# Optimization experiments

Measured on AMD Instinct MI355X. Metric: run time of the kernel, lower is better.

## Reference

```python
import jax, jax.numpy as jnp
import numpy as np

B, N, F, NCG, NCONV, VOCAB = 16, 1024, 128, 64, 3, 100
EPS = 0.001


def setup_inputs() -> dict:
    key = jax.random.key(0)
    ks = jax.random.split(key, 16)
    atoms_nodes = jax.random.randint(ks[0], (B, N), 0, VOCAB, dtype=jnp.int32)
    xyz = jax.random.normal(ks[1], (B, N, 3), jnp.float32) * 3.0
    # chain bonds (i, i+1) per molecule -> every atom has degree >= 1
    bi = jnp.repeat(jnp.arange(B), N - 1)
    si = jnp.tile(jnp.arange(N - 1), B)
    bonds = jnp.stack([bi, si, si + 1], axis=1).astype(jnp.int32)  # [B*(N-1), 3]
    tau = jnp.float32(1.0)
    gumbel_u = jax.random.uniform(ks[2], (B, N, NCG), jnp.float32, 1e-6, 1.0 - 1e-6)
    # parameters
    emb = jax.random.normal(ks[3], (VOCAB, F), jnp.float32) * 0.1
    emb = emb.at[0].set(0.0)  # padding_idx=0
    s = 1.0 / np.sqrt(F)
    upd_W1 = jax.random.uniform(ks[4], (NCONV, F, F), jnp.float32, -s, s)
    upd_b1 = jax.random.uniform(ks[5], (NCONV, F), jnp.float32, -s, s)
    upd_W2 = jax.random.uniform(ks[6], (NCONV, F, F), jnp.float32, -s, s)
    upd_b2 = jax.random.uniform(ks[7], (NCONV, F), jnp.float32, -s, s)
    cg_W1 = jax.random.uniform(ks[8], (F, F), jnp.float32, -s, s)
    cg_b1 = jax.random.uniform(ks[9], (F,), jnp.float32, -s, s)
    cg_W2 = jax.random.uniform(ks[10], (F, NCG), jnp.float32, -s, s)
    cg_b2 = jax.random.uniform(ks[11], (NCG,), jnp.float32, -s, s)
    return {"atoms_nodes": atoms_nodes, "xyz": xyz, "bonds": bonds, "tau": tau,
            "gumbel_u": gumbel_u, "emb": emb,
            "upd_W1": upd_W1, "upd_b1": upd_b1, "upd_W2": upd_W2, "upd_b2": upd_b2,
            "cg_W1": cg_W1, "cg_b1": cg_b1, "cg_W2": cg_W2, "cg_b2": cg_b2}


def reference(atoms_nodes, xyz, bonds, tau, gumbel_u, emb,
              upd_W1, upd_b1, upd_W2, upd_b2, cg_W1, cg_b1, cg_W2, cg_b2):
    h = emb[atoms_nodes]  # [B,N,F]
    # dense symmetric adjacency from bond list
    adj = jnp.zeros((B, N, N), jnp.float32)
    adj = adj.at[bonds[:, 0], bonds[:, 1], bonds[:, 2]].set(1.0)
    adj = adj.at[bonds[:, 0], bonds[:, 2], bonds[:, 1]].set(1.0)
    deg = jnp.sum(adj, axis=-1)[:, :, None]  # [B,N,1]
    for l in range(NCONV):
        ch = jnp.tanh(h @ upd_W1[l] + upd_b1[l]) @ upd_W2[l] + upd_b2[l]
        dh = jnp.einsum('bif,bij->bjf', ch, adj) / deg
        h = h + dh
    # gumbel-softmax assignment (soft)
    assign_logits = jnp.tanh(h @ cg_W1 + cg_b1) @ cg_W2 + cg_b2  # [B,N,NCG]
    g = -jnp.log(-jnp.log(gumbel_u))
    M = jax.nn.softmax((assign_logits + g) / tau, axis=-1)  # [B,N,NCG]
    M_norm = M / jnp.sum(M, axis=-2, keepdims=True)
    H = jnp.einsum('bnj,bnf->bjf', M_norm, h)        # [B,NCG,F]
    cg_xyz = jnp.einsum('bin,bij->bjn', xyz, M_norm)  # [B,NCG,3]
    cg_adj = jnp.broadcast_to(jnp.ones((NCG, NCG)) - jnp.eye(NCG), (B, NCG, NCG))
    diff = cg_xyz[:, :, None, :] - cg_xyz[:, None, :, :]
    dist = jnp.sqrt(jnp.sum(diff * diff, axis=-1) + EPS)  # [B,NCG,NCG]
    knbrs = jnp.argsort(dist, axis=-1)
    return (M, M_norm, h, H, adj, cg_xyz, cg_adj, knbrs)
```

## Files before the change

kernel.cpp:

```cpp
#include <hip/hip_runtime.h>
#include <math.h>

#define BB 16
#define NN 1024
#define FF 128
#define NCG 64
#define NCONV 3
#define CAP 8

static const size_t O_M     = 0;
static const size_t O_MN    = (size_t)BB*NN*NCG;
static const size_t O_H     = O_MN  + (size_t)BB*NN*NCG;
static const size_t O_HH    = O_H   + (size_t)BB*NN*FF;
static const size_t O_ADJ   = O_HH  + (size_t)BB*NCG*FF;
static const size_t O_CGXYZ = O_ADJ + (size_t)BB*NN*NN;
static const size_t O_CGADJ = O_CGXYZ + (size_t)BB*NCG*3;
static const size_t O_KN    = O_CGADJ + (size_t)BB*NCG*NCG;

static const size_t S_H64   = 0;
static const size_t S_T64   = 2097152;
static const size_t S_C64   = 4194304;
static const size_t S_LM64  = 0;
static const size_t S_COLSP = 4194304;
static const size_t S_HPF   = 6291456;
static const size_t S_CGP   = 6815744;
static const size_t S_NBR   = 6840320;
static const size_t S_W64   = 6905856;

static const size_t WO_CGW1 = 98304;
static const size_t WO_CGW2 = 114688;
static const int    W64_N   = 122880;

static const size_t W_INVD = 0;
static const size_t W_COLS = (size_t)BB*NN;
static const size_t W_CG64 = W_COLS + (size_t)BB*NCG;
static const size_t W_CNT  = W_CG64 + (size_t)BB*NCG*3;

__global__ void k_zero(int* cnt) {
    int i = blockIdx.x * blockDim.x + threadIdx.x;
    if (i < BB*NN) cnt[i] = 0;
}

__global__ void k_build_nbr(const int* __restrict__ bonds, int nb, int* cnt, int* nbr) {
    int i = blockIdx.x * blockDim.x + threadIdx.x;
    if (i >= nb) return;
    int b = bonds[i*3+0], s = bonds[i*3+1], t = bonds[i*3+2];
    int ns = b*NN + s, nt = b*NN + t;
    int p = atomicAdd(&cnt[ns], 1);
    if (p < CAP) nbr[(size_t)ns*CAP + p] = nt;
    int q = atomicAdd(&cnt[nt], 1);
    if (q < CAP) nbr[(size_t)nt*CAP + q] = ns;
}

__global__ void k_invdeg(const int* __restrict__ cnt, double* invdeg) {
    int i = blockIdx.x * blockDim.x + threadIdx.x;
    if (i >= BB*NN) return;
    int d = cnt[i];
    invdeg[i] = d > 0 ? 1.0 / (double)d : 0.0;
}

__global__ void k_cgadj(float* cgadj) {
    int idx = blockIdx.x * blockDim.x + threadIdx.x;
    if (idx >= BB*NCG*NCG) return;
    int i = (idx / NCG) % NCG, j = idx % NCG;
    cgadj[idx] = (i == j) ? 0.f : 1.f;
}

__global__ void k_emb64(const int* __restrict__ atoms, const float* __restrict__ emb,
                        double* __restrict__ h) {
    int idx = blockIdx.x * blockDim.x + threadIdx.x;
    if (idx >= BB*NN*(FF/4)) return;
    int n = idx / (FF/4), f4 = idx % (FF/4);
    int a = atoms[n];
    const float4 v = *reinterpret_cast<const float4*>(&emb[(size_t)a*FF + f4*4]);
    double* hp = &h[(size_t)n*FF + f4*4];
    hp[0] = (double)v.x; hp[1] = (double)v.y; hp[2] = (double)v.z; hp[3] = (double)v.w;
}

__global__ void k_cvtW(const float* __restrict__ uW1, const float* __restrict__ uW2,
                       const float* __restrict__ cgW1, const float* __restrict__ cgW2,
                       double* __restrict__ W64) {
    int idx = blockIdx.x * blockDim.x + threadIdx.x;
    if (idx >= W64_N) return;
    float v;
    if (idx < 98304) {
        int l = idx >> 15, r = idx & 32767;
        v = (r < 16384) ? uW1[l*16384 + r] : uW2[l*16384 + (r & 16383)];
    } else if (idx < 114688) {
        v = cgW1[idx - 98304];
    } else {
        v = cgW2[idx - 114688];
    }
    W64[idx] = (double)v;
}

template<int COUTT, bool TANH>
__global__ __launch_bounds__(256) void k_gemm64(const double* __restrict__ in,
                                                const double* __restrict__ W,
                                                const float* __restrict__ bias,
                                                double* __restrict__ out) {
    constexpr int K = 128, KC = 32;
    constexpr int CT2 = COUTT/2;
    __shared__ double As[64*34];
    __shared__ double Ws[KC*64];
    const int tid = threadIdx.x;
    const int col0 = blockIdx.y * 64;
    const int C02 = col0 >> 1;
    const size_t row0 = (size_t)blockIdx.x * 64;
    const double2* in2 = reinterpret_cast<const double2*>(in + row0*K);
    const double2* Wg2 = reinterpret_cast<const double2*>(W);
    double2* As2 = reinterpret_cast<double2*>(As);
    double2* Ws2 = reinterpret_cast<double2*>(Ws);

    double2 pA[4], pW[4];
    #pragma unroll
    for (int i = 0; i < 4; ++i) { int q = tid + i*256; pA[i] = in2[(q>>4)*64 + (q&15)]; }
    #pragma unroll
    for (int i = 0; i < 4; ++i) { int q = tid + i*256; pW[i] = Wg2[(q>>5)*CT2 + C02 + (q&31)]; }

    const int tc = tid & 15, tr = tid >> 4;
    double acc[4][4];
    #pragma unroll
    for (int i = 0; i < 4; ++i)
        #pragma unroll
        for (int j = 0; j < 4; ++j) acc[i][j] = 0.0;

    for (int kc = 0; kc < K; kc += KC) {
        __syncthreads();
        #pragma unroll
        for (int i = 0; i < 4; ++i) { int q = tid + i*256; As2[(q>>4)*17 + (q&15)] = pA[i]; }
        #pragma unroll
        for (int i = 0; i < 4; ++i) { int q = tid + i*256; Ws2[(q>>5)*32 + (q&31)] = pW[i]; }
        if (kc + KC < K) {
            const int kn = kc + KC, kn2 = kn >> 1;
            #pragma unroll
            for (int i = 0; i < 4; ++i) { int q = tid + i*256; pA[i] = in2[(q>>4)*64 + kn2 + (q&15)]; }
            #pragma unroll
            for (int i = 0; i < 4; ++i) { int q = tid + i*256; pW[i] = Wg2[(kn + (q>>5))*CT2 + C02 + (q&31)]; }
        }
        __syncthreads();
        #pragma unroll
        for (int kk2 = 0; kk2 < KC/2; ++kk2) {
            double2 a[4];
            #pragma unroll
            for (int i = 0; i < 4; ++i) a[i] = As2[(tr + 16*i)*17 + kk2];
            const double2* w0 = Ws2 + (2*kk2+0)*32;
            const double2* w1 = Ws2 + (2*kk2+1)*32;
            #pragma unroll
            for (int g = 0; g < 2; ++g) {
                double2 u0 = w0[tc + g*16];
                double2 u1 = w1[tc + g*16];
                #pragma unroll
                for (int i = 0; i < 4; ++i) {
                    acc[i][g*2+0] += a[i].x*u0.x + a[i].y*u1.x;
                    acc[i][g*2+1] += a[i].x*u0.y + a[i].y*u1.y;
                }
            }
        }
    }

    #pragma unroll
    for (int g = 0; g < 2; ++g) {
        int c = col0 + tc*2 + g*32;
        double b0 = (double)bias[c], b1 = (double)bias[c+1];
        #pragma unroll
        for (int i = 0; i < 4; ++i) {
            double2 o;
            o.x = acc[i][g*2+0] + b0;
            o.y = acc[i][g*2+1] + b1;
            if (TANH) { o.x = tanh(o.x); o.y = tanh(o.y); }
            *reinterpret_cast<double2*>(&out[(row0 + tr + 16*i)*COUTT + c]) = o;
        }
    }
}

template<bool WRITE_F32>
__global__ void k_gather(const double* __restrict__ ch, const double* __restrict__ invdeg,
                         const int* __restrict__ nbr, const int* __restrict__ cnt,
                         double* __restrict__ h, float* __restrict__ hout) {
    int idx = blockIdx.x * blockDim.x + threadIdx.x;
    if (idx >= BB*NN*(FF/4)) return;
    int node = idx >> 5, f4 = idx & 31;
    int c = cnt[node];
    double2 s0; s0.x = 0.0; s0.y = 0.0;
    double2 s1 = s0;
    for (int q = 0; q < c; ++q) {
        int nb = nbr[(size_t)node*CAP + q];
        const double2* cp = reinterpret_cast<const double2*>(ch + (size_t)nb*FF + f4*4);
        double2 a = cp[0], b2 = cp[1];
        s0.x += a.x; s0.y += a.y; s1.x += b2.x; s1.y += b2.y;
    }
    double w = invdeg[node];
    double2* hp = reinterpret_cast<double2*>(h + (size_t)node*FF + f4*4);
    double2 h0 = hp[0], h1 = hp[1];
    h0.x += s0.x*w; h0.y += s0.y*w; h1.x += s1.x*w; h1.y += s1.y*w;
    hp[0] = h0; hp[1] = h1;
    if (WRITE_F32) {
        float4 o; o.x = (float)h0.x; o.y = (float)h0.y; o.z = (float)h1.x; o.w = (float)h1.y;
        *reinterpret_cast<float4*>(&hout[(size_t)node*FF + f4*4]) = o;
    }
}

__global__ void k_softmax64(double* __restrict__ lm, const float* __restrict__ gum,
                            const float* __restrict__ tau_p, float* __restrict__ M_out) {
    int row = blockIdx.x * 4 + threadIdx.x / 64;
    int lane = threadIdx.x & 63;
    double tau = (double)(*tau_p);
    double u = (double)gum[(size_t)row*NCG + lane];
    double g = -log(-log(u));
    double v = (lm[(size_t)row*NCG + lane] + g) / tau;
    double m = v;
    #pragma unroll
    for (int off = 32; off; off >>= 1) m = fmax(m, __shfl_xor(m, off));
    double e = exp(v - m);
    double s = e;
    #pragma unroll
    for (int off = 32; off; off >>= 1) s += __shfl_xor(s, off);
    double mv = e / s;
    lm[(size_t)row*NCG + lane] = mv;
    M_out[(size_t)row*NCG + lane] = (float)mv;
}

__global__ __launch_bounds__(256) void k_cols_part(const double* __restrict__ M,
                                                   double* __restrict__ colsp) {
    __shared__ double red[256];
    const int b = blockIdx.x, c = blockIdx.y;
    const int tid = threadIdx.x;
    const int j = tid & 63, q = tid >> 6;
    const double* Mb = M + (size_t)b*NN*NCG + (size_t)(c*64 + q*16)*NCG;
    double s = 0.0;
    #pragma unroll
    for (int r = 0; r < 16; ++r) s += Mb[(size_t)r*NCG + j];
    red[tid] = s;
    __syncthreads();
    if (tid < 64)
        colsp[((size_t)b*16 + c)*NCG + j] = red[j] + red[64+j] + red[128+j] + red[192+j];
}

__global__ void k_cols_fin(const double* __restrict__ colsp, double* __restrict__ colsum) {
    int idx = blockIdx.x * blockDim.x + threadIdx.x;
    if (idx >= BB*NCG) return;
    int b = idx >> 6, j = idx & 63;
    double s = 0.0;
    #pragma unroll
    for (int c = 0; c < 16; ++c) s += colsp[((size_t)b*16 + c)*NCG + j];
    colsum[idx] = s;
}

__global__ void k_mnorm_out(const double* __restrict__ M, const double* __restrict__ colsum,
                            float* __restrict__ Mn) {
    size_t i = (size_t)blockIdx.x * blockDim.x + threadIdx.x;
    if (i >= (size_t)BB*NN*NCG) return;
    size_t b = i >> 16;
    int j = (int)(i & 63);
    Mn[i] = (float)(M[i] / colsum[b*NCG + j]);
}

__global__ __launch_bounds__(256) void k_Hpart32(const float* __restrict__ Mn,
                                                 const float* __restrict__ h,
                                                 float* __restrict__ Hp) {
    __shared__ float Ms[32*NCG];
    __shared__ float hs[32*FF];
    const int b = blockIdx.x, ch = blockIdx.y;
    const int tid = threadIdx.x;
    const int tc = tid % 32, tr = tid / 32;
    const float4* M4 = reinterpret_cast<const float4*>(Mn + (size_t)b*NN*NCG);
    const float4* h4 = reinterpret_cast<const float4*>(h + (size_t)b*NN*FF);
    float4* Ms4 = reinterpret_cast<float4*>(Ms);
    float4* hs4 = reinterpret_cast<float4*>(hs);
    const float2* Ms2 = reinterpret_cast<const float2*>(Ms);
    const float2* hs2 = reinterpret_cast<const float2*>(hs);

    float acc[8][4];
    #pragma unroll
    for (int i = 0; i < 8; ++i)
        #pragma unroll
        for (int j = 0; j < 4; ++j) acc[i][j] = 0.f;

    for (int s = 0; s < 4; ++s) {
        const int n0 = ch*128 + s*32;
        __syncthreads();
        #pragma unroll
        for (int i = 0; i < 2; ++i) Ms4[tid + i*256] = M4[n0*16 + tid + i*256];
        #pragma unroll
        for (int i = 0; i < 4; ++i) hs4[tid + i*256] = h4[n0*32 + tid + i*256];
        __syncthreads();
        for (int n = 0; n < 32; ++n) {
            float2 hv0 = hs2[n*64 + tc];
            float2 hv1 = hs2[n*64 + 32 + tc];
            float2 m0 = Ms2[n*32 + tr];
            float2 m1 = Ms2[n*32 + 8 + tr];
            float2 m2 = Ms2[n*32 + 16 + tr];
            float2 m3 = Ms2[n*32 + 24 + tr];
            float mj[8] = {m0.x, m0.y, m1.x, m1.y, m2.x, m2.y, m3.x, m3.y};
            #pragma unroll
            for (int jj = 0; jj < 8; ++jj) {
                acc[jj][0] += mj[jj]*hv0.x; acc[jj][1] += mj[jj]*hv0.y;
                acc[jj][2] += mj[jj]*hv1.x; acc[jj][3] += mj[jj]*hv1.y;
            }
        }
    }
    float* Ho = Hp + ((size_t)ch*BB + b) * NCG * FF;
    #pragma unroll
    for (int gj = 0; gj < 4; ++gj)
        #pragma unroll
        for (int pj = 0; pj < 2; ++pj) {
            int j = tr*2 + gj*16 + pj;
            int jj = gj*2 + pj;
            float2 o0; o0.x = acc[jj][0]; o0.y = acc[jj][1];
            float2 o1; o1.x = acc[jj][2]; o1.y = acc[jj][3];
            float2* op = reinterpret_cast<float2*>(Ho + (size_t)j*FF);
            op[tc] = o0; op[32 + tc] = o1;
        }
}

__global__ void k_Hfin32(const float* __restrict__ Hp, float* __restrict__ H) {
    int idx = blockIdx.x * blockDim.x + threadIdx.x;
    if (idx >= BB*NCG*FF) return;
    int b = idx / (NCG*FF);
    int r = idx % (NCG*FF);
    float s = 0.f;
    #pragma unroll
    for (int c = 0; c < 8; ++c) s += Hp[((size_t)c*BB + b)*NCG*FF + r];
    H[idx] = s;
}

__global__ __launch_bounds__(192) void k_cgpart(const double* __restrict__ M,
                                                const float* __restrict__ xyz,
                                                double* __restrict__ cgp) {
    __shared__ double Ms[32*NCG];
    __shared__ double xs[32*3];
    const int b = blockIdx.x, ch = blockIdx.y;
    const int tid = threadIdx.x;
    const int j = tid / 3, d = tid % 3;
    const double2* M2 = reinterpret_cast<const double2*>(M + (size_t)b*NN*NCG);
    double2* Ms2 = reinterpret_cast<double2*>(Ms);
    const float* xb = xyz + (size_t)b*NN*3;
    double acc = 0.0;
    for (int s = 0; s < 4; ++s) {
        const int n0 = ch*128 + s*32;
        __syncthreads();
        for (int q = tid; q < 1024; q += 192) Ms2[q] = M2[n0*32 + q];
        for (int q = tid; q < 96; q += 192) xs[q] = (double)xb[n0*3 + q];
        __syncthreads();
        for (int n = 0; n < 32; ++n)
            acc += Ms[n*NCG + j] * xs[n*3 + d];
    }
    cgp[((size_t)ch*BB + b)*NCG*3 + tid] = acc;
}

__global__ void k_cgfin(const double* __restrict__ cgp, const double* __restrict__ colsum,
                        double* __restrict__ cg64, float* __restrict__ cg) {
    int idx = blockIdx.x * blockDim.x + threadIdx.x;
    if (idx >= BB*NCG*3) return;
    int b = idx / (NCG*3);
    int r = idx % (NCG*3);
    int j = r / 3;
    double s = 0.0;
    #pragma unroll
    for (int c = 0; c < 8; ++c) s += cgp[((size_t)c*BB + b)*NCG*3 + r];
    double v = s / colsum[b*NCG + j];
    cg64[idx] = v;
    cg[idx] = (float)v;
}

__global__ __launch_bounds__(1024) void k_knbrs(const double* __restrict__ cg,
                                                float* __restrict__ kn) {
    __shared__ double cs[NCG*3];
    const int b = blockIdx.x;
    const int tid = threadIdx.x;
    const int i = blockIdx.y * 16 + tid / 64;
    const int j = tid & 63;
    if (tid < NCG*3) cs[tid] = cg[(size_t)b*NCG*3 + tid];
    __syncthreads();
    double xi = cs[i*3+0], yi = cs[i*3+1], zi = cs[i*3+2];
    double dxj = xi - cs[j*3+0], dyj = yi - cs[j*3+1], dzj = zi - cs[j*3+2];
    double d2j = dxj*dxj + dyj*dyj + dzj*dzj;
    int rank = 0;
    for (int k = 0; k < NCG; ++k) {
        double dx = xi - cs[k*3+0], dy = yi - cs[k*3+1], dz = zi - cs[k*3+2];
        double d2k = dx*dx + dy*dy + dz*dz;
        rank += (d2k < d2j) || (d2k == d2j && k < j);
    }
    kn[(size_t)b*NCG*NCG + (size_t)i*NCG + rank] = (float)j;
}

__global__ void k_zero_adj(float4* adj4, long n4) {
    long i = (long)blockIdx.x * blockDim.x + threadIdx.x;
    long stride = (long)gridDim.x * blockDim.x;
    float4 z; z.x = z.y = z.z = z.w = 0.f;
    for (; i < n4; i += stride) adj4[i] = z;
}

__global__ void k_bonds_adj(const int* __restrict__ bonds, int nb, float* adj) {
    int i = blockIdx.x * blockDim.x + threadIdx.x;
    if (i >= nb) return;
    int b = bonds[i*3+0], s = bonds[i*3+1], t = bonds[i*3+2];
    size_t base = (size_t)b * NN * NN;
    adj[base + (size_t)s*NN + t] = 1.f;
    adj[base + (size_t)t*NN + s] = 1.f;
}

extern "C" void kernel_launch(void* const* d_in, const int* in_sizes, int n_in,
                              void* d_out, int out_size, void* d_ws, size_t ws_size,
                              hipStream_t stream) {
    const int*   atoms  = (const int*)  d_in[0];
    const float* xyz    = (const float*)d_in[1];
    const int*   bonds  = (const int*)  d_in[2];
    const float* tau    = (const float*)d_in[3];
    const float* gum    = (const float*)d_in[4];
    const float* emb    = (const float*)d_in[5];
    const float* uW1    = (const float*)d_in[6];
    const float* ub1    = (const float*)d_in[7];
    const float* uW2    = (const float*)d_in[8];
    const float* ub2    = (const float*)d_in[9];
    const float* cgW1   = (const float*)d_in[10];
    const float* cgb1   = (const float*)d_in[11];
    const float* cgW2   = (const float*)d_in[12];
    const float* cgb2   = (const float*)d_in[13];

    float* out = (float*)d_out;
    float* o_M   = out + O_M;
    float* o_Mn  = out + O_MN;
    float* o_h   = out + O_H;
    float* o_H   = out + O_HH;
    float* o_adj = out + O_ADJ;
    float* o_cg  = out + O_CGXYZ;
    float* o_ca  = out + O_CGADJ;
    float* o_kn  = out + O_KN;

    double* scr   = (double*)o_adj;
    double* h64   = scr + S_H64;
    double* t64   = scr + S_T64;
    double* c64   = scr + S_C64;
    double* lm64  = scr + S_LM64;
    double* colsp = scr + S_COLSP;
    float*  Hpf   = (float*)(scr + S_HPF);
    double* cgp   = scr + S_CGP;
    int*    nbr   = (int*)(scr + S_NBR);
    double* W64   = scr + S_W64;

    double* wsd    = (double*)d_ws;
    double* invdeg = wsd + W_INVD;
    double* colsum = wsd + W_COLS;
    double* cg64   = wsd + W_CG64;
    int*    cnt    = (int*)(wsd + W_CNT);

    const int nb = in_sizes[2] / 3;

    hipLaunchKernelGGL(k_zero, dim3(64), dim3(256), 0, stream, cnt);
    hipLaunchKernelGGL(k_build_nbr, dim3((nb+255)/256), dim3(256), 0, stream,
                       bonds, nb, cnt, nbr);
    hipLaunchKernelGGL(k_invdeg, dim3(64), dim3(256), 0, stream, cnt, invdeg);
    hipLaunchKernelGGL(k_cgadj, dim3(256), dim3(256), 0, stream, o_ca);
    hipLaunchKernelGGL(k_cvtW, dim3((W64_N+255)/256), dim3(256), 0, stream,
                       uW1, uW2, cgW1, cgW2, W64);
    hipLaunchKernelGGL(k_emb64, dim3(2048), dim3(256), 0, stream, atoms, emb, h64);

    for (int l = 0; l < NCONV; ++l) {
        hipLaunchKernelGGL((k_gemm64<128,true>), dim3(256,2), dim3(256), 0, stream,
                           h64, W64 + (size_t)l*32768, ub1 + (size_t)l*FF, t64);
        hipLaunchKernelGGL((k_gemm64<128,false>), dim3(256,2), dim3(256), 0, stream,
                           t64, W64 + (size_t)l*32768 + 16384, ub2 + (size_t)l*FF, c64);
        if (l < NCONV-1)
            hipLaunchKernelGGL((k_gather<false>), dim3(2048), dim3(256), 0, stream,
                               c64, invdeg, nbr, cnt, h64, o_h);
        else
            hipLaunchKernelGGL((k_gather<true>), dim3(2048), dim3(256), 0, stream,
                               c64, invdeg, nbr, cnt, h64, o_h);
    }

    hipLaunchKernelGGL((k_gemm64<128,true>), dim3(256,2), dim3(256), 0, stream,
                       h64, W64 + WO_CGW1, cgb1, t64);
    hipLaunchKernelGGL((k_gemm64<64,false>), dim3(256,1), dim3(256), 0, stream,
                       t64, W64 + WO_CGW2, cgb2, lm64);

    hipLaunchKernelGGL(k_softmax64, dim3(4096), dim3(256), 0, stream,
                       lm64, gum, tau, o_M);
    hipLaunchKernelGGL(k_cols_part, dim3(16,16), dim3(256), 0, stream, lm64, colsp);
    hipLaunchKernelGGL(k_cols_fin, dim3(4), dim3(256), 0, stream, colsp, colsum);
    hipLaunchKernelGGL(k_mnorm_out, dim3(4096), dim3(256), 0, stream, lm64, colsum, o_Mn);
    hipLaunchKernelGGL(k_Hpart32, dim3(BB, 8), dim3(256), 0, stream, o_Mn, o_h, Hpf);
    hipLaunchKernelGGL(k_Hfin32, dim3(512), dim3(256), 0, stream, Hpf, o_H);
    hipLaunchKernelGGL(k_cgpart, dim3(BB, 8), dim3(192), 0, stream, lm64, xyz, cgp);
    hipLaunchKernelGGL(k_cgfin, dim3(12), dim3(256), 0, stream, cgp, colsum, cg64, o_cg);
    hipLaunchKernelGGL(k_knbrs, dim3(BB, 4), dim3(1024), 0, stream, cg64, o_kn);

    hipLaunchKernelGGL(k_zero_adj, dim3(4096), dim3(256), 0, stream,
                       (float4*)o_adj, (long)BB*NN*NN/4);
    hipLaunchKernelGGL(k_bonds_adj, dim3((nb+255)/256), dim3(256), 0, stream,
                       bonds, nb, o_adj);
}
```

Before: 399.8 us.

## Use FP64 MFMA for dense GEMMs and widen split-K for H and cg_xyz

Replaces the scalar FP64 register-tiled GEMM with a kernel built on the 16x16x4 FP64 MFMA instruction, padding the weight tile in shared memory to reduce bank conflicts. The k_Hpart32 reduction and cg_xyz partial-sum kernels are split over more node chunks (16 and 32), with more blocks per kernel and longer final reductions; scratch offsets move to fit the larger partial buffers. The aim is to raise GEMM throughput and fill more CUs in the small reduction kernels, at the cost of more partial-sum traffic and scalar rather than vector output stores.

```diff
diff --git a/kernel.cpp b/kernel.cpp
--- a/kernel.cpp
+++ b/kernel.cpp
@@ -7,6 +7,8 @@
 #define NCG 64
 #define NCONV 3
 #define CAP 8
+
+typedef double f64x4 __attribute__((ext_vector_type(4)));
 
 static const size_t O_M     = 0;
 static const size_t O_MN    = (size_t)BB*NN*NCG;
@@ -23,9 +25,9 @@
 static const size_t S_LM64  = 0;
 static const size_t S_COLSP = 4194304;
 static const size_t S_HPF   = 6291456;
-static const size_t S_CGP   = 6815744;
-static const size_t S_NBR   = 6840320;
-static const size_t S_W64   = 6905856;
+static const size_t S_CGP   = 7340032;
+static const size_t S_NBR   = 7438336;
+static const size_t S_W64   = 7503872;
 
 static const size_t WO_CGW1 = 98304;
 static const size_t WO_CGW2 = 114688;
@@ -95,14 +97,14 @@
 }
 
 template<int COUTT, bool TANH>
-__global__ __launch_bounds__(256) void k_gemm64(const double* __restrict__ in,
-                                                const double* __restrict__ W,
-                                                const float* __restrict__ bias,
-                                                double* __restrict__ out) {
+__global__ __launch_bounds__(256) void k_gemm_mfma(const double* __restrict__ in,
+                                                   const double* __restrict__ W,
+                                                   const float* __restrict__ bias,
+                                                   double* __restrict__ out) {
     constexpr int K = 128, KC = 32;
     constexpr int CT2 = COUTT/2;
     __shared__ double As[64*34];
-    __shared__ double Ws[KC*64];
+    __shared__ double Ws[KC*66];
     const int tid = threadIdx.x;
     const int col0 = blockIdx.y * 64;
     const int C02 = col0 >> 1;
@@ -118,19 +120,21 @@
     #pragma unroll
     for (int i = 0; i < 4; ++i) { int q = tid + i*256; pW[i] = Wg2[(q>>5)*CT2 + C02 + (q&31)]; }
 
-    const int tc = tid & 15, tr = tid >> 4;
-    double acc[4][4];
-    #pragma unroll
-    for (int i = 0; i < 4; ++i)
-        #pragma unroll
-        for (int j = 0; j < 4; ++j) acc[i][j] = 0.0;
+    const int lane = tid & 63;
+    const int wv = tid >> 6;
+    const int m = lane & 15, kq = lane >> 4;
+    const int arow = (wv*16 + m)*34 + kq;
+
+    f64x4 acc[4];
+    #pragma unroll
+    for (int ct = 0; ct < 4; ++ct) acc[ct] = (f64x4){0.0, 0.0, 0.0, 0.0};
 
     for (int kc = 0; kc < K; kc += KC) {
         __syncthreads();
         #pragma unroll
         for (int i = 0; i < 4; ++i) { int q = tid + i*256; As2[(q>>4)*17 + (q&15)] = pA[i]; }
         #pragma unroll
-        for (int i = 0; i < 4; ++i) { int q = tid + i*256; Ws2[(q>>5)*32 + (q&31)] = pW[i]; }
+        for (int i = 0; i < 4; ++i) { int q = tid + i*256; Ws2[(q>>5)*33 + (q&31)] = pW[i]; }
         if (kc + KC < K) {
             const int kn = kc + KC, kn2 = kn >> 1;
             #pragma unroll
@@ -140,36 +144,27 @@
         }
         __syncthreads();
         #pragma unroll
-        for (int kk2 = 0; kk2 < KC/2; ++kk2) {
-            double2 a[4];
+        for (int kk = 0; kk < KC; kk += 4) {
+            double a = As[arow + kk];
+            const double* wrow = Ws + (kk + kq)*66 + m;
             #pragma unroll
-            for (int i = 0; i < 4; ++i) a[i] = As2[(tr + 16*i)*17 + kk2];
-            const double2* w0 = Ws2 + (2*kk2+0)*32;
-            const double2* w1 = Ws2 + (2*kk2+1)*32;
-            #pragma unroll
-            for (int g = 0; g < 2; ++g) {
-                double2 u0 = w0[tc + g*16];
-                double2 u1 = w1[tc + g*16];
-                #pragma unroll
-                for (int i = 0; i < 4; ++i) {
-                    acc[i][g*2+0] += a[i].x*u0.x + a[i].y*u1.x;
-                    acc[i][g*2+1] += a[i].x*u0.y + a[i].y*u1.y;
-                }
+            for (int ct = 0; ct < 4; ++ct) {
+                double b = wrow[ct*16];
+                acc[ct] = __builtin_amdgcn_mfma_f64_16x16x4f64(a, b, acc[ct], 0, 0, 0);
             }
         }
     }
 
-    #pragma unroll
-    for (int g = 0; g < 2; ++g) {
-        int c = col0 + tc*2 + g*32;
-        double b0 = (double)bias[c], b1 = (double)bias[c+1];
+    const int orow = wv*16 + kq*4;
+    #pragma unroll
+    for (int ct = 0; ct < 4; ++ct) {
+        int c = col0 + ct*16 + m;
+        double bv = (double)bias[c];
         #pragma unroll
         for (int i = 0; i < 4; ++i) {
-            double2 o;
-            o.x = acc[i][g*2+0] + b0;
-            o.y = acc[i][g*2+1] + b1;
-            if (TANH) { o.x = tanh(o.x); o.y = tanh(o.y); }
-            *reinterpret_cast<double2*>(&out[(row0 + tr + 16*i)*COUTT + c]) = o;
+            double v = acc[ct][i] + bv;
+            if (TANH) v = tanh(v);
+            out[(row0 + orow + i)*COUTT + c] = v;
         }
     }
 }
@@ -277,8 +272,8 @@
         #pragma unroll
         for (int j = 0; j < 4; ++j) acc[i][j] = 0.f;
 
-    for (int s = 0; s < 4; ++s) {
-        const int n0 = ch*128 + s*32;
+    for (int s = 0; s < 2; ++s) {
+        const int n0 = ch*64 + s*32;
         __syncthreads();
         #pragma unroll
         for (int i = 0; i < 2; ++i) Ms4[tid + i*256] = M4[n0*16 + tid + i*256];
@@ -321,7 +316,7 @@
     int r = idx % (NCG*FF);
     float s = 0.f;
     #pragma unroll
-    for (int c = 0; c < 8; ++c) s += Hp[((size_t)c*BB + b)*NCG*FF + r];
+    for (int c = 0; c < 16; ++c) s += Hp[((size_t)c*BB + b)*NCG*FF + r];
     H[idx] = s;
 }
 
@@ -333,20 +328,17 @@
     const int b = blockIdx.x, ch = blockIdx.y;
     const int tid = threadIdx.x;
     const int j = tid / 3, d = tid % 3;
+    const int n0 = ch*32;
     const double2* M2 = reinterpret_cast<const double2*>(M + (size_t)b*NN*NCG);
     double2* Ms2 = reinterpret_cast<double2*>(Ms);
     const float* xb = xyz + (size_t)b*NN*3;
+    for (int q = tid; q < 1024; q += 192) Ms2[q] = M2[n0*32 + q];
+    for (int q = tid; q < 96; q += 192) xs[q] = (double)xb[n0*3 + q];
+    __syncthreads();
     double acc = 0.0;
-    for (int s = 0; s < 4; ++s) {
-        const int n0 = ch*128 + s*32;
-        __syncthreads();
-        for (int q = tid; q < 1024; q += 192) Ms2[q] = M2[n0*32 + q];
-        for (int q = tid; q < 96; q += 192) xs[q] = (double)xb[n0*3 + q];
-        __syncthreads();
-        for (int n = 0; n < 32; ++n)
-            acc += Ms[n*NCG + j] * xs[n*3 + d];
-    }
-    cgp[((size_t)ch*BB + b)*NCG*3 + tid] = acc;
+    #pragma unroll 8
+    for (int n = 0; n < 32; ++n) acc += Ms[n*NCG + j] * xs[n*3 + d];
+    cgp[((size_t)ch*BB + b)*192 + tid] = acc;
 }
 
 __global__ void k_cgfin(const double* __restrict__ cgp, const double* __restrict__ colsum,
@@ -358,7 +350,7 @@
     int j = r / 3;
     double s = 0.0;
     #pragma unroll
-    for (int c = 0; c < 8; ++c) s += cgp[((size_t)c*BB + b)*NCG*3 + r];
+    for (int c = 0; c < 32; ++c) s += cgp[((size_t)c*BB + b)*192 + r];
     double v = s / colsum[b*NCG + j];
     cg64[idx] = v;
     cg[idx] = (float)v;
@@ -458,9 +450,9 @@
     hipLaunchKernelGGL(k_emb64, dim3(2048), dim3(256), 0, stream, atoms, emb, h64);
 
     for (int l = 0; l < NCONV; ++l) {
-        hipLaunchKernelGGL((k_gemm64<128,true>), dim3(256,2), dim3(256), 0, stream,
+        hipLaunchKernelGGL((k_gemm_mfma<128,true>), dim3(256,2), dim3(256), 0, stream,
                            h64, W64 + (size_t)l*32768, ub1 + (size_t)l*FF, t64);
-        hipLaunchKernelGGL((k_gemm64<128,false>), dim3(256,2), dim3(256), 0, stream,
+        hipLaunchKernelGGL((k_gemm_mfma<128,false>), dim3(256,2), dim3(256), 0, stream,
                            t64, W64 + (size_t)l*32768 + 16384, ub2 + (size_t)l*FF, c64);
         if (l < NCONV-1)
             hipLaunchKernelGGL((k_gather<false>), dim3(2048), dim3(256), 0, stream,
@@ -470,9 +462,9 @@
                                c64, invdeg, nbr, cnt, h64, o_h);
     }
 
-    hipLaunchKernelGGL((k_gemm64<128,true>), dim3(256,2), dim3(256), 0, stream,
+    hipLaunchKernelGGL((k_gemm_mfma<128,true>), dim3(256,2), dim3(256), 0, stream,
                        h64, W64 + WO_CGW1, cgb1, t64);
-    hipLaunchKernelGGL((k_gemm64<64,false>), dim3(256,1), dim3(256), 0, stream,
+    hipLaunchKernelGGL((k_gemm_mfma<64,false>), dim3(256,1), dim3(256), 0, stream,
                        t64, W64 + WO_CGW2, cgb2, lm64);
 
     hipLaunchKernelGGL(k_softmax64, dim3(4096), dim3(256), 0, stream,
@@ -480,9 +472,9 @@
     hipLaunchKernelGGL(k_cols_part, dim3(16,16), dim3(256), 0, stream, lm64, colsp);
     hipLaunchKernelGGL(k_cols_fin, dim3(4), dim3(256), 0, stream, colsp, colsum);
     hipLaunchKernelGGL(k_mnorm_out, dim3(4096), dim3(256), 0, stream, lm64, colsum, o_Mn);
-    hipLaunchKernelGGL(k_Hpart32, dim3(BB, 8), dim3(256), 0, stream, o_Mn, o_h, Hpf);
+    hipLaunchKernelGGL(k_Hpart32, dim3(BB, 16), dim3(256), 0, stream, o_Mn, o_h, Hpf);
     hipLaunchKernelGGL(k_Hfin32, dim3(512), dim3(256), 0, stream, Hpf, o_H);
-    hipLaunchKernelGGL(k_cgpart, dim3(BB, 8), dim3(192), 0, stream, lm64, xyz, cgp);
+    hipLaunchKernelGGL(k_cgpart, dim3(BB, 32), dim3(192), 0, stream, lm64, xyz, cgp);
     hipLaunchKernelGGL(k_cgfin, dim3(12), dim3(256), 0, stream, cgp, colsum, cg64, o_cg);
     hipLaunchKernelGGL(k_knbrs, dim3(BB, 4), dim3(1024), 0, stream, cg64, o_kn);
 
```

Measured after the change: 369.8 us. 7.5% less time.
